# Kernel optimization log

Hardware: AMD Instinct MI355X
Metric: run time of the kernel (lower is better)

The kernel has to match this reference:

```python
import jax, jax.numpy as jnp
import numpy as np

N_ATOMS = 200000
N_EDGES = 800000
ATOM_FDIM = 133
HIDDEN = 256
NUM_MOLS = 8000
ALPHA = 0.2  # LeakyReLU slope


def setup_inputs() -> dict:
    key = jax.random.key(0)
    ks = jax.random.split(key, 10)
    f_atoms = jax.random.normal(ks[0], (N_ATOMS, ATOM_FDIM), dtype=jnp.float32)
    edge_index = jax.random.randint(ks[1], (2, N_EDGES), 0, N_ATOMS, dtype=jnp.int64)
    mol_ids = jnp.sort(jax.random.randint(ks[2], (N_ATOMS,), 0, NUM_MOLS, dtype=jnp.int64))
    s0 = 1.0 / np.sqrt(ATOM_FDIM)
    sh = 1.0 / np.sqrt(HIDDEN)
    sa = 1.0 / np.sqrt(2 * HIDDEN)
    W0 = jax.random.normal(ks[3], (ATOM_FDIM, HIDDEN), dtype=jnp.float32) * s0
    a0 = jax.random.normal(ks[4], (2 * HIDDEN,), dtype=jnp.float32) * sa
    W1 = jax.random.normal(ks[5], (HIDDEN, HIDDEN), dtype=jnp.float32) * sh
    a1 = jax.random.normal(ks[6], (2 * HIDDEN,), dtype=jnp.float32) * sa
    W2 = jax.random.normal(ks[7], (HIDDEN, HIDDEN), dtype=jnp.float32) * sh
    a2 = jax.random.normal(ks[8], (2 * HIDDEN,), dtype=jnp.float32) * sa
    return {"f_atoms": f_atoms, "edge_index": edge_index, "mol_ids": mol_ids,
            "W0": W0, "a0": a0, "W1": W1, "a1": a1, "W2": W2, "a2": a2}


def _gat_layer(x, W, a, src, tgt, residual):
    # x: [N, Fin], W: [Fin, H], a: [2H]
    h = x @ W                              # [N, H]
    H = h.shape[1]
    a_s, a_t = a[:H], a[H:]
    # e = leakyrelu([h_src || h_tgt] @ a), computed without materializing the concat
    e = jax.nn.leaky_relu(h[src] @ a_s + h[tgt] @ a_t, negative_slope=ALPHA)  # [E]
    att = jnp.exp(e)
    denom = jax.ops.segment_sum(att, tgt, num_segments=x.shape[0])            # [N]
    att_n = att / (denom[tgt] + 1e-8)
    # weighted scatter-aggregate (dropout is a no-op in eval mode)
    h_prime = jax.ops.segment_sum(h[src] * att_n[:, None], tgt, num_segments=x.shape[0])
    if residual:
        h_prime = h_prime + x
    return jax.nn.elu(h_prime)


def reference(f_atoms, edge_index, mol_ids, W0, a0, W1, a1, W2, a2):
    src, tgt = edge_index[0], edge_index[1]
    x = _gat_layer(f_atoms, W0, a0, src, tgt, residual=False)
    x = _gat_layer(x, W1, a1, src, tgt, residual=True)
    x = _gat_layer(x, W2, a2, src, tgt, residual=True)
    # per-molecule mean pooling (a_scope loop -> segment mean)
    sums = jax.ops.segment_sum(x, mol_ids, num_segments=NUM_MOLS)            # [M, H]
    counts = jax.ops.segment_sum(jnp.ones((x.shape[0],), x.dtype), mol_ids, num_segments=NUM_MOLS)
    return jnp.where(counts[:, None] > 0, sums / jnp.maximum(counts[:, None], 1.0), 0.0)
```

## Files before the change

kernel.cpp:

```cpp
#include <hip/hip_runtime.h>

#define N_ATOMS 200000
#define N_EDGES 800000
#define FDIM    133
#define HID     256
#define NMOLS   8000
#define CAP     32

typedef unsigned short bf16_t;
typedef __attribute__((ext_vector_type(4))) float f32x4;
typedef __attribute__((ext_vector_type(8))) short bf16x8;

__device__ inline float bf2f(bf16_t u) {
    union { unsigned int i; float f; } v; v.i = ((unsigned int)u) << 16; return v.f;
}
__device__ inline bf16_t f2bf(float f) {
    union { float f; unsigned int i; } v; v.f = f;
    return (bf16_t)((v.i + 0x7fffu + ((v.i >> 16) & 1u)) >> 16);
}
__device__ inline float4 ld4(const bf16_t* p) {
    ushort4 u = *(const ushort4*)p;
    return make_float4(bf2f(u.x), bf2f(u.y), bf2f(u.z), bf2f(u.w));
}
__device__ inline void st4(bf16_t* p, float4 v) {
    ushort4 u; u.x = f2bf(v.x); u.y = f2bf(v.y); u.z = f2bf(v.z); u.w = f2bf(v.w);
    *(ushort4*)p = u;
}

__device__ inline void gload_lds16(const void* g, void* l) {
    __builtin_amdgcn_global_load_lds((const __attribute__((address_space(1))) unsigned int*)g,
                                     (__attribute__((address_space(3))) unsigned int*)l,
                                     16, 0, 0);
}

__global__ __launch_bounds__(256) void build_adj(const int* __restrict__ ei,
                                                 int* __restrict__ cnt,
                                                 int* __restrict__ lst) {
    int e = blockIdx.x * 256 + threadIdx.x;
    if (e >= N_EDGES) return;
    int s = ei[e];
    int t = ei[N_EDGES + e];
    int p = atomicAdd(&cnt[t], 1);
    if (p < CAP) lst[t * CAP + p] = s;
}

__global__ __launch_bounds__(256) void transpose_w(const float* __restrict__ W,
                                                   bf16_t* __restrict__ Wt,
                                                   int K, int Kpad) {
    int idx = blockIdx.x * 256 + threadIdx.x;
    if (idx >= HID * Kpad) return;
    int n = idx / Kpad, k = idx - n * Kpad;
    Wt[idx] = (k < K) ? f2bf(W[k * HID + n]) : (bf16_t)0;
}

template <bool A_FP32, int KSTEPS, int LDA>
__global__ __launch_bounds__(256) void gemm_mfma(const void* __restrict__ Av,
                                                 const bf16_t* __restrict__ Wt,
                                                 bf16_t* __restrict__ H,
                                                 const float* __restrict__ avec,
                                                 float* __restrict__ ssp,
                                                 float* __restrict__ stp) {
    __shared__ bf16_t As[2][128][32];
    __shared__ bf16_t Bs[2][128][32];
    const int tid  = threadIdx.x;
    const int lane = tid & 63;
    const int w    = tid >> 6;
    const int wr   = w >> 1, wc = w & 1;
    const int row0 = blockIdx.x * 128;
    const int n0   = blockIdx.y * 128;
    const int KP   = KSTEPS * 32;

    const long long slot = (long long)(blockIdx.y * 2 + wc) * N_ATOMS;
    ssp += slot;
    stp += slot;

    float sreg[16];
    const int sr  = tid >> 1;
    const int skh = (tid & 1) * 16;
    int sgrow = row0 + sr; if (sgrow >= N_ATOMS) sgrow = N_ATOMS - 1;

#define ISSUE(ks_, buf_) do {                                                          \
    const int k0_ = (ks_) * 32;                                                        \
    if constexpr (A_FP32) {                                                            \
        _Pragma("unroll")                                                              \
        for (int j = 0; j < 16; ++j) {                                                 \
            int gk = k0_ + skh + j;                                                    \
            sreg[j] = (gk < LDA) ? ((const float*)Av)[(long long)sgrow * LDA + gk] : 0.f; \
        }                                                                              \
    } else {                                                                           \
        _Pragma("unroll")                                                              \
        for (int j = 0; j < 2; ++j) {                                                  \
            int u = j * 4096 + w * 1024 + lane * 16;                                   \
            int r = u >> 6, cb = u & 63;                                               \
            int grow = row0 + r; if (grow >= N_ATOMS) grow = N_ATOMS - 1;              \
            gload_lds16((const bf16_t*)Av + (long long)grow * LDA + k0_ + (cb >> 1),   \
                        (char*)&As[buf_][0][0] + j * 4096 + w * 1024);                 \
        }                                                                              \
    }                                                                                  \
    _Pragma("unroll")                                                                  \
    for (int j = 0; j < 2; ++j) {                                                      \
        int u = j * 4096 + w * 1024 + lane * 16;                                       \
        int r = u >> 6, cb = u & 63;                                                   \
        gload_lds16(Wt + (long long)(n0 + r) * KP + k0_ + (cb >> 1),                   \
                    (char*)&Bs[buf_][0][0] + j * 4096 + w * 1024);                     \
    }                                                                                  \
} while (0)

#define COMMIT(buf_) do {                                                              \
    if constexpr (A_FP32) {                                                            \
        short v_[16];                                                                  \
        _Pragma("unroll")                                                              \
        for (int j = 0; j < 16; ++j) v_[j] = (short)f2bf(sreg[j]);                     \
        *(bf16x8*)&As[buf_][sr][skh]     = *(bf16x8*)&v_[0];                           \
        *(bf16x8*)&As[buf_][sr][skh + 8] = *(bf16x8*)&v_[8];                           \
    }                                                                                  \
} while (0)

    f32x4 acc[4][4] = {};

    ISSUE(0, 0);
    COMMIT(0);
    __syncthreads();

    int buf = 0;
    #pragma unroll
    for (int ks = 0; ks < KSTEPS; ++ks) {
        if (ks + 1 < KSTEPS) ISSUE(ks + 1, buf ^ 1);

        const int fr   = lane & 15;
        const int koff = (lane >> 4) * 8;
        bf16x8 af[4], bfr[4];
        #pragma unroll
        for (int i = 0; i < 4; ++i)
            af[i] = *(const bf16x8*)&As[buf][wr * 64 + i * 16 + fr][koff];
        #pragma unroll
        for (int jn = 0; jn < 4; ++jn)
            bfr[jn] = *(const bf16x8*)&Bs[buf][wc * 64 + jn * 16 + fr][koff];
        #pragma unroll
        for (int i = 0; i < 4; ++i)
            #pragma unroll
            for (int jn = 0; jn < 4; ++jn)
                acc[i][jn] = __builtin_amdgcn_mfma_f32_16x16x32_bf16(af[i], bfr[jn], acc[i][jn], 0, 0, 0);

        if (ks + 1 < KSTEPS) COMMIT(buf ^ 1);
        __syncthreads();
        buf ^= 1;
    }
#undef ISSUE
#undef COMMIT

    float as_v[4], at_v[4];
    #pragma unroll
    for (int jn = 0; jn < 4; ++jn) {
        int c = n0 + wc * 64 + jn * 16 + (lane & 15);
        as_v[jn] = avec[c];
        at_v[jn] = avec[HID + c];
    }
    #pragma unroll
    for (int i = 0; i < 4; ++i) {
        #pragma unroll
        for (int rr = 0; rr < 4; ++rr) {
            int r = row0 + wr * 64 + i * 16 + (lane >> 4) * 4 + rr;
            float ps = 0.f, pt = 0.f;
            #pragma unroll
            for (int jn = 0; jn < 4; ++jn) {
                float h = acc[i][jn][rr];
                ps += h * as_v[jn];
                pt += h * at_v[jn];
                if (r < N_ATOMS)
                    H[(long long)r * HID + (n0 + wc * 64 + jn * 16 + (lane & 15))] = f2bf(h);
            }
            #pragma unroll
            for (int o = 1; o < 16; o <<= 1) {
                ps += __shfl_xor(ps, o);
                pt += __shfl_xor(pt, o);
            }
            if ((lane & 15) == 0 && r < N_ATOMS) {
                ssp[r] = ps;
                stp[r] = pt;
            }
        }
    }
}

__global__ __launch_bounds__(256) void combine_dots(const float* __restrict__ ssp,
                                                    const float* __restrict__ stp,
                                                    float* __restrict__ ss,
                                                    float* __restrict__ st) {
    int i = blockIdx.x * 256 + threadIdx.x;
    if (i >= N_ATOMS) return;
    ss[i] = (ssp[i] + ssp[N_ATOMS + i]) + (ssp[2 * N_ATOMS + i] + ssp[3 * N_ATOMS + i]);
    st[i] = (stp[i] + stp[N_ATOMS + i]) + (stp[2 * N_ATOMS + i] + stp[3 * N_ATOMS + i]);
}

__global__ __launch_bounds__(256) void aggregate(const bf16_t* __restrict__ H,
                                                 const float* __restrict__ ss,
                                                 const float* __restrict__ st,
                                                 const int* __restrict__ cnt,
                                                 const int* __restrict__ lst,
                                                 bf16_t* __restrict__ X,
                                                 int residual) {
    int wave = threadIdx.x >> 6;
    int lane = threadIdx.x & 63;
    int t = blockIdx.x * 4 + wave;
    if (t >= N_ATOMS) return;
    int n = cnt[t]; if (n > CAP) n = CAP;
    float stt = st[t];
    const int base = t * CAP;

    float ax = 0.f, ay = 0.f, az = 0.f, aw = 0.f;
    float denom = 0.f;

    for (int i0 = 0; i0 < n; i0 += 4) {
        int4 s4 = *(const int4*)&lst[base + i0];
        int s0 = (i0 + 0 < n) ? s4.x : t;
        int s1 = (i0 + 1 < n) ? s4.y : t;
        int s2 = (i0 + 2 < n) ? s4.z : t;
        int s3 = (i0 + 3 < n) ? s4.w : t;

        float v0 = ss[s0], v1 = ss[s1], v2 = ss[s2], v3 = ss[s3];

        float e0 = v0 + stt; e0 = e0 > 0.f ? e0 : 0.2f * e0;
        float e1 = v1 + stt; e1 = e1 > 0.f ? e1 : 0.2f * e1;
        float e2 = v2 + stt; e2 = e2 > 0.f ? e2 : 0.2f * e2;
        float e3 = v3 + stt; e3 = e3 > 0.f ? e3 : 0.2f * e3;

        float t0 = (i0 + 0 < n) ? __expf(e0) : 0.f;
        float t1 = (i0 + 1 < n) ? __expf(e1) : 0.f;
        float t2 = (i0 + 2 < n) ? __expf(e2) : 0.f;
        float t3 = (i0 + 3 < n) ? __expf(e3) : 0.f;

        float4 h0 = ld4(&H[(long long)s0 * HID + lane * 4]);
        float4 h1 = ld4(&H[(long long)s1 * HID + lane * 4]);
        float4 h2 = ld4(&H[(long long)s2 * HID + lane * 4]);
        float4 h3 = ld4(&H[(long long)s3 * HID + lane * 4]);

        denom += (t0 + t1) + (t2 + t3);
        ax += t0 * h0.x + t1 * h1.x + t2 * h2.x + t3 * h3.x;
        ay += t0 * h0.y + t1 * h1.y + t2 * h2.y + t3 * h3.y;
        az += t0 * h0.z + t1 * h1.z + t2 * h2.z + t3 * h3.z;
        aw += t0 * h0.w + t1 * h1.w + t2 * h2.w + t3 * h3.w;
    }

    float inv = 1.f / (denom + 1e-8f);
    float rx = ax * inv, ry = ay * inv, rz = az * inv, rw = aw * inv;
    if (residual) {
        float4 xv = ld4(&X[(long long)t * HID + lane * 4]);
        rx += xv.x; ry += xv.y; rz += xv.z; rw += xv.w;
    }
    rx = rx > 0.f ? rx : (__expf(rx) - 1.f);
    ry = ry > 0.f ? ry : (__expf(ry) - 1.f);
    rz = rz > 0.f ? rz : (__expf(rz) - 1.f);
    rw = rw > 0.f ? rw : (__expf(rw) - 1.f);
    st4(&X[(long long)t * HID + lane * 4], make_float4(rx, ry, rz, rw));
}

__device__ inline int lower_bound_i(const int* a, int n, int v) {
    int lo = 0, hi = n;
    while (lo < hi) { int mid = (lo + hi) >> 1; if (a[mid] < v) lo = mid + 1; else hi = mid; }
    return lo;
}

__global__ __launch_bounds__(64) void pool_kernel(const bf16_t* __restrict__ X,
                                                  const int* __restrict__ mol,
                                                  float* __restrict__ out) {
    int m = blockIdx.x;
    int lane = threadIdx.x;
    int lo = lower_bound_i(mol, N_ATOMS, m);
    int hi = lower_bound_i(mol, N_ATOMS, m + 1);
    float ax = 0.f, ay = 0.f, az = 0.f, aw = 0.f;
    for (int i = lo; i < hi; ++i) {
        float4 v = ld4(&X[(long long)i * HID + lane * 4]);
        ax += v.x; ay += v.y; az += v.z; aw += v.w;
    }
    float c = (float)(hi - lo);
    float4 r = make_float4(0.f, 0.f, 0.f, 0.f);
    if (c > 0.f) {
        float inv = 1.f / c;
        r = make_float4(ax * inv, ay * inv, az * inv, aw * inv);
    }
    *(float4*)&out[(long long)m * HID + lane * 4] = r;
}

extern "C" void kernel_launch(void* const* d_in, const int* in_sizes, int n_in,
                              void* d_out, int out_size, void* d_ws, size_t ws_size,
                              hipStream_t stream) {
    const float* f_atoms = (const float*)d_in[0];
    const int*   ei      = (const int*)d_in[1];
    const int*   mol     = (const int*)d_in[2];
    const float* W0      = (const float*)d_in[3];
    const float* a0      = (const float*)d_in[4];
    const float* W1      = (const float*)d_in[5];
    const float* a1      = (const float*)d_in[6];
    const float* W2      = (const float*)d_in[7];
    const float* a2      = (const float*)d_in[8];
    float* out = (float*)d_out;

    char* ws = (char*)d_ws;
    size_t off = 0;
    bf16_t* X  = (bf16_t*)(ws + off); off += (size_t)N_ATOMS * HID * 2;
    bf16_t* Hb = (bf16_t*)(ws + off); off += (size_t)N_ATOMS * HID * 2;
    float* ss  = (float*)(ws + off);  off += (size_t)N_ATOMS * 4;
    float* st  = (float*)(ws + off);  off += (size_t)N_ATOMS * 4;
    int* cnt   = (int*)(ws + off);    off += (size_t)N_ATOMS * 4;
    int* lst   = (int*)(ws + off);    off += (size_t)N_ATOMS * CAP * 4;
    if (ws_size < off) return;

    char* ob = (char*)d_out;
    bf16_t* Wt  = (bf16_t*)ob;
    float*  ssp = (float*)(ob + 131072);
    float*  stp = (float*)(ob + 131072 + 3200000);

    hipMemsetAsync(cnt, 0, (size_t)N_ATOMS * 4, stream);
    build_adj<<<(N_EDGES + 255) / 256, 256, 0, stream>>>(ei, cnt, lst);

    const dim3 gemm_grid((N_ATOMS + 127) / 128, 2);
    const int  agg_blocks = N_ATOMS / 4;
    const int  cmb_blocks = (N_ATOMS + 255) / 256;

    transpose_w<<<(HID * 160 + 255) / 256, 256, 0, stream>>>(W0, Wt, FDIM, 160);
    gemm_mfma<true, 5, FDIM><<<gemm_grid, 256, 0, stream>>>(f_atoms, Wt, Hb, a0, ssp, stp);
    combine_dots<<<cmb_blocks, 256, 0, stream>>>(ssp, stp, ss, st);
    aggregate<<<agg_blocks, 256, 0, stream>>>(Hb, ss, st, cnt, lst, X, 0);

    transpose_w<<<(HID * HID + 255) / 256, 256, 0, stream>>>(W1, Wt, HID, HID);
    gemm_mfma<false, 8, HID><<<gemm_grid, 256, 0, stream>>>(X, Wt, Hb, a1, ssp, stp);
    combine_dots<<<cmb_blocks, 256, 0, stream>>>(ssp, stp, ss, st);
    aggregate<<<agg_blocks, 256, 0, stream>>>(Hb, ss, st, cnt, lst, X, 1);

    transpose_w<<<(HID * HID + 255) / 256, 256, 0, stream>>>(W2, Wt, HID, HID);
    gemm_mfma<false, 8, HID><<<gemm_grid, 256, 0, stream>>>(X, Wt, Hb, a2, ssp, stp);
    combine_dots<<<cmb_blocks, 256, 0, stream>>>(ssp, stp, ss, st);
    aggregate<<<agg_blocks, 256, 0, stream>>>(Hb, ss, st, cnt, lst, X, 1);

    pool_kernel<<<NMOLS, 64, 0, stream>>>(X, mol, out);
}
```

Baseline: 666.7 us.

## Replace LDS-tiled MFMA GEMM with direct global-to-register fragment loads

The GEMM drops its double-buffered LDS staging and loads A and B MFMA fragments straight from global memory into registers. Each block now covers 64 rows and all 256 columns, with each wave owning 64 columns, so the A rows are shared across waves only through cache. The goal is to remove LDS traffic, barriers and the 2-D grid, but global loads are now uncoalesced 16-byte fragment reads with no software pipelining, and the fp32 path issues strided scalar loads.

```diff
diff --git a/kernel.cpp b/kernel.cpp
--- a/kernel.cpp
+++ b/kernel.cpp
@@ -25,12 +25,6 @@
 __device__ inline void st4(bf16_t* p, float4 v) {
     ushort4 u; u.x = f2bf(v.x); u.y = f2bf(v.y); u.z = f2bf(v.z); u.w = f2bf(v.w);
     *(ushort4*)p = u;
-}
-
-__device__ inline void gload_lds16(const void* g, void* l) {
-    __builtin_amdgcn_global_load_lds((const __attribute__((address_space(1))) unsigned int*)g,
-                                     (__attribute__((address_space(3))) unsigned int*)l,
-                                     16, 0, 0);
 }
 
 __global__ __launch_bounds__(256) void build_adj(const int* __restrict__ ei,
@@ -53,106 +47,63 @@
     Wt[idx] = (k < K) ? f2bf(W[k * HID + n]) : (bf16_t)0;
 }
 
-template <bool A_FP32, int KSTEPS, int LDA>
-__global__ __launch_bounds__(256) void gemm_mfma(const void* __restrict__ Av,
-                                                 const bf16_t* __restrict__ Wt,
-                                                 bf16_t* __restrict__ H,
-                                                 const float* __restrict__ avec,
-                                                 float* __restrict__ ssp,
-                                                 float* __restrict__ stp) {
-    __shared__ bf16_t As[2][128][32];
-    __shared__ bf16_t Bs[2][128][32];
+template <bool A_FP32, int KSTEPS, int LDA, int KP>
+__global__ __launch_bounds__(256) void gemm_direct(const void* __restrict__ Av,
+                                                   const bf16_t* __restrict__ Wt,
+                                                   bf16_t* __restrict__ H,
+                                                   const float* __restrict__ avec,
+                                                   float* __restrict__ ssp,
+                                                   float* __restrict__ stp) {
     const int tid  = threadIdx.x;
     const int lane = tid & 63;
     const int w    = tid >> 6;
-    const int wr   = w >> 1, wc = w & 1;
-    const int row0 = blockIdx.x * 128;
-    const int n0   = blockIdx.y * 128;
-    const int KP   = KSTEPS * 32;
-
-    const long long slot = (long long)(blockIdx.y * 2 + wc) * N_ATOMS;
-    ssp += slot;
-    stp += slot;
-
-    float sreg[16];
-    const int sr  = tid >> 1;
-    const int skh = (tid & 1) * 16;
-    int sgrow = row0 + sr; if (sgrow >= N_ATOMS) sgrow = N_ATOMS - 1;
-
-#define ISSUE(ks_, buf_) do {                                                          \
-    const int k0_ = (ks_) * 32;                                                        \
-    if constexpr (A_FP32) {                                                            \
-        _Pragma("unroll")                                                              \
-        for (int j = 0; j < 16; ++j) {                                                 \
-            int gk = k0_ + skh + j;                                                    \
-            sreg[j] = (gk < LDA) ? ((const float*)Av)[(long long)sgrow * LDA + gk] : 0.f; \
-        }                                                                              \
-    } else {                                                                           \
-        _Pragma("unroll")                                                              \
-        for (int j = 0; j < 2; ++j) {                                                  \
-            int u = j * 4096 + w * 1024 + lane * 16;                                   \
-            int r = u >> 6, cb = u & 63;                                               \
-            int grow = row0 + r; if (grow >= N_ATOMS) grow = N_ATOMS - 1;              \
-            gload_lds16((const bf16_t*)Av + (long long)grow * LDA + k0_ + (cb >> 1),   \
-                        (char*)&As[buf_][0][0] + j * 4096 + w * 1024);                 \
-        }                                                                              \
-    }                                                                                  \
-    _Pragma("unroll")                                                                  \
-    for (int j = 0; j < 2; ++j) {                                                      \
-        int u = j * 4096 + w * 1024 + lane * 16;                                       \
-        int r = u >> 6, cb = u & 63;                                                   \
-        gload_lds16(Wt + (long long)(n0 + r) * KP + k0_ + (cb >> 1),                   \
-                    (char*)&Bs[buf_][0][0] + j * 4096 + w * 1024);                     \
-    }                                                                                  \
-} while (0)
-
-#define COMMIT(buf_) do {                                                              \
-    if constexpr (A_FP32) {                                                            \
-        short v_[16];                                                                  \
-        _Pragma("unroll")                                                              \
-        for (int j = 0; j < 16; ++j) v_[j] = (short)f2bf(sreg[j]);                     \
-        *(bf16x8*)&As[buf_][sr][skh]     = *(bf16x8*)&v_[0];                           \
-        *(bf16x8*)&As[buf_][sr][skh + 8] = *(bf16x8*)&v_[8];                           \
-    }                                                                                  \
-} while (0)
+    const int fr   = lane & 15;
+    const int kg   = lane >> 4;
+    const int row0 = blockIdx.x * 64;
+    const int col0 = w * 64;
+
+    ssp += (long long)w * N_ATOMS;
+    stp += (long long)w * N_ATOMS;
 
     f32x4 acc[4][4] = {};
 
-    ISSUE(0, 0);
-    COMMIT(0);
-    __syncthreads();
-
-    int buf = 0;
-    #pragma unroll
+    #pragma unroll 2
     for (int ks = 0; ks < KSTEPS; ++ks) {
-        if (ks + 1 < KSTEPS) ISSUE(ks + 1, buf ^ 1);
-
-        const int fr   = lane & 15;
-        const int koff = (lane >> 4) * 8;
+        const int kbase = ks * 32 + kg * 8;
         bf16x8 af[4], bfr[4];
+
+        if constexpr (A_FP32) {
+            const float* A = (const float*)Av;
+            #pragma unroll
+            for (int i = 0; i < 4; ++i) {
+                const float* src = A + (long long)(row0 + i * 16 + fr) * LDA + kbase;
+                short v[8];
+                #pragma unroll
+                for (int j = 0; j < 8; ++j)
+                    v[j] = (kbase + j < LDA) ? (short)f2bf(src[j]) : (short)0;
+                af[i] = *(bf16x8*)v;
+            }
+        } else {
+            const bf16_t* A = (const bf16_t*)Av;
+            #pragma unroll
+            for (int i = 0; i < 4; ++i)
+                af[i] = *(const bf16x8*)(A + (long long)(row0 + i * 16 + fr) * LDA + kbase);
+        }
+        #pragma unroll
+        for (int jn = 0; jn < 4; ++jn)
+            bfr[jn] = *(const bf16x8*)(Wt + (long long)(col0 + jn * 16 + fr) * KP + kbase);
+
         #pragma unroll
         for (int i = 0; i < 4; ++i)
-            af[i] = *(const bf16x8*)&As[buf][wr * 64 + i * 16 + fr][koff];
-        #pragma unroll
-        for (int jn = 0; jn < 4; ++jn)
-            bfr[jn] = *(const bf16x8*)&Bs[buf][wc * 64 + jn * 16 + fr][koff];
-        #pragma unroll
-        for (int i = 0; i < 4; ++i)
             #pragma unroll
             for (int jn = 0; jn < 4; ++jn)
                 acc[i][jn] = __builtin_amdgcn_mfma_f32_16x16x32_bf16(af[i], bfr[jn], acc[i][jn], 0, 0, 0);
-
-        if (ks + 1 < KSTEPS) COMMIT(buf ^ 1);
-        __syncthreads();
-        buf ^= 1;
-    }
-#undef ISSUE
-#undef COMMIT
+    }
 
     float as_v[4], at_v[4];
     #pragma unroll
     for (int jn = 0; jn < 4; ++jn) {
-        int c = n0 + wc * 64 + jn * 16 + (lane & 15);
+        int c = col0 + jn * 16 + fr;
         as_v[jn] = avec[c];
         at_v[jn] = avec[HID + c];
     }
@@ -160,22 +111,21 @@
     for (int i = 0; i < 4; ++i) {
         #pragma unroll
         for (int rr = 0; rr < 4; ++rr) {
-            int r = row0 + wr * 64 + i * 16 + (lane >> 4) * 4 + rr;
+            int r = row0 + i * 16 + kg * 4 + rr;
             float ps = 0.f, pt = 0.f;
             #pragma unroll
             for (int jn = 0; jn < 4; ++jn) {
                 float h = acc[i][jn][rr];
                 ps += h * as_v[jn];
                 pt += h * at_v[jn];
-                if (r < N_ATOMS)
-                    H[(long long)r * HID + (n0 + wc * 64 + jn * 16 + (lane & 15))] = f2bf(h);
+                H[(long long)r * HID + (col0 + jn * 16 + fr)] = f2bf(h);
             }
             #pragma unroll
             for (int o = 1; o < 16; o <<= 1) {
                 ps += __shfl_xor(ps, o);
                 pt += __shfl_xor(pt, o);
             }
-            if ((lane & 15) == 0 && r < N_ATOMS) {
+            if (fr == 0) {
                 ssp[r] = ps;
                 stp[r] = pt;
             }
@@ -314,22 +264,22 @@
     hipMemsetAsync(cnt, 0, (size_t)N_ATOMS * 4, stream);
     build_adj<<<(N_EDGES + 255) / 256, 256, 0, stream>>>(ei, cnt, lst);
 
-    const dim3 gemm_grid((N_ATOMS + 127) / 128, 2);
-    const int  agg_blocks = N_ATOMS / 4;
-    const int  cmb_blocks = (N_ATOMS + 255) / 256;
+    const int gemm_blocks = N_ATOMS / 64;
+    const int agg_blocks  = N_ATOMS / 4;
+    const int cmb_blocks  = (N_ATOMS + 255) / 256;
 
     transpose_w<<<(HID * 160 + 255) / 256, 256, 0, stream>>>(W0, Wt, FDIM, 160);
-    gemm_mfma<true, 5, FDIM><<<gemm_grid, 256, 0, stream>>>(f_atoms, Wt, Hb, a0, ssp, stp);
+    gemm_direct<true, 5, FDIM, 160><<<gemm_blocks, 256, 0, stream>>>(f_atoms, Wt, Hb, a0, ssp, stp);
     combine_dots<<<cmb_blocks, 256, 0, stream>>>(ssp, stp, ss, st);
     aggregate<<<agg_blocks, 256, 0, stream>>>(Hb, ss, st, cnt, lst, X, 0);
 
     transpose_w<<<(HID * HID + 255) / 256, 256, 0, stream>>>(W1, Wt, HID, HID);
-    gemm_mfma<false, 8, HID><<<gemm_grid, 256, 0, stream>>>(X, Wt, Hb, a1, ssp, stp);
+    gemm_direct<false, 8, HID, HID><<<gemm_blocks, 256, 0, stream>>>(X, Wt, Hb, a1, ssp, stp);
     combine_dots<<<cmb_blocks, 256, 0, stream>>>(ssp, stp, ss, st);
     aggregate<<<agg_blocks, 256, 0, stream>>>(Hb, ss, st, cnt, lst, X, 1);
 
     transpose_w<<<(HID * HID + 255) / 256, 256, 0, stream>>>(W2, Wt, HID, HID);
-    gemm_mfma<false, 8, HID><<<gemm_grid, 256, 0, stream>>>(X, Wt, Hb, a2, ssp, stp);
+    gemm_direct<false, 8, HID, HID><<<gemm_blocks, 256, 0, stream>>>(X, Wt, Hb, a2, ssp, stp);
     combine_dots<<<cmb_blocks, 256, 0, stream>>>(ssp, stp, ss, st);
     aggregate<<<agg_blocks, 256, 0, stream>>>(Hb, ss, st, cnt, lst, X, 1);
 
```

Result: slower. 767.6 us (+15.1%).
